# Performance work log

Hardware: AMD Instinct MI355X
Metric: run time of the kernel (lower is better)

## Reference

```python
import jax, jax.numpy as jnp
import numpy as np

EPS = 1e-6


def setup_inputs() -> dict:
    key = jax.random.key(0)
    ks = jax.random.split(key, 7)
    T, B, D, n, r = 512, 32, 1024, 1024, 8
    x = jax.random.normal(ks[0], (T, B, D), dtype=jnp.float32)
    # xavier_uniform-like init for weights
    def xavier(k, shape):
        fan_in, fan_out = shape[1], shape[0]
        a = float(np.sqrt(6.0 / (fan_in + fan_out)))
        return jax.random.uniform(k, shape, dtype=jnp.float32, minval=-a, maxval=a)
    W_k = xavier(ks[1], (n, D))
    W_v = xavier(ks[2], (n, D))
    W_q = xavier(ks[3], (n, D))
    W_kr = xavier(ks[4], (r, n))
    U0 = jnp.zeros((B, n, r), dtype=jnp.float32)
    V0 = jax.random.normal(ks[5], (B, n, r), dtype=jnp.float32) * 0.01
    return {"x": x, "W_k": W_k, "W_v": W_v, "W_q": W_q, "W_kr": W_kr, "U0": U0, "V0": V0}


def reference(x, W_k, W_v, W_q, W_kr, U0, V0):
    # x: [T, B, D]; state S = U @ V^T with U,V: [B, n, r]
    k = jnp.einsum('tbd,nd->tbn', x, W_k)
    v = jnp.einsum('tbd,nd->tbn', x, W_v)
    q = jnp.einsum('tbd,nd->tbn', x, W_q)
    V = V0  # V is never updated in the recurrence

    def step(U, kvq):
        k_t, v_t, q_t = kvq  # each [B, n]
        k_norm = k_t / (jnp.linalg.norm(k_t, axis=-1, keepdims=True) + EPS)
        Vtk = jnp.einsum('bnr,bn->br', V, k_norm)
        retrieved = jnp.einsum('bnr,br->bn', U, Vtk)
        delta = v_t - retrieved
        k_r = k_norm @ W_kr.T  # [B, r]
        U_new = jnp.tanh(U + delta[:, :, None] * k_r[:, None, :])
        Vtq = jnp.einsum('bnr,bn->br', V, q_t)
        Sq = jnp.einsum('bnr,br->bn', U_new, Vtq)
        out = Sq * jax.nn.silu(Sq)
        return U_new, out

    U_final, output = jax.lax.scan(step, U0, (k, v, q))
    return output, (U_final, V)
```

## Files before the change

kernel.cpp:

```cpp
#include <hip/hip_runtime.h>
#include <hip/hip_bf16.h>

typedef __attribute__((ext_vector_type(8))) short short8;
typedef __attribute__((ext_vector_type(4))) short short4v;
typedef __attribute__((ext_vector_type(4))) float f32x4;
typedef __attribute__((ext_vector_type(2))) float f32x2;
typedef unsigned short u16;

__device__ inline float b2f(u16 u) {
    unsigned int i = ((unsigned int)u) << 16;
    float f; __builtin_memcpy(&f, &i, 4); return f;
}
__device__ inline u16 f2b(float f) {
    unsigned int i; __builtin_memcpy(&i, &f, 4);
    unsigned int r = (i + 0x7FFFu + ((i >> 16) & 1u)) >> 16;
    return (u16)r;
}

__device__ inline float xsum32(float x) {
    unsigned u; __builtin_memcpy(&u, &x, 4);
    auto r = __builtin_amdgcn_permlane32_swap(u, u, false, false);
    unsigned s0 = r[0], s1 = r[1];
    float f0, f1; __builtin_memcpy(&f0, &s0, 4); __builtin_memcpy(&f1, &s1, 4);
    return f0 + f1;
}

__device__ inline float xsum16(float x) {
#if __has_builtin(__builtin_amdgcn_permlane16_swap)
    unsigned u; __builtin_memcpy(&u, &x, 4);
    auto r = __builtin_amdgcn_permlane16_swap(u, u, false, false);
    unsigned s0 = r[0], s1 = r[1];
    float f0, f1; __builtin_memcpy(&f0, &s0, 4); __builtin_memcpy(&f1, &s1, 4);
    return f0 + f1;
#else
    return x + __shfl_xor(x, 16, 64);
#endif
}

#define GLDS(g, l) __builtin_amdgcn_global_load_lds( \
    (const __attribute__((address_space(1))) void*)(g), \
    (__attribute__((address_space(3))) void*)(l), 16, 0, 0)

#define KWAIT(N) asm volatile("s_waitcnt lgkmcnt(0)\n\t" \
                              "s_waitcnt vmcnt(" #N ")\n\t" \
                              "s_barrier" ::: "memory")

__global__ __launch_bounds__(256) void cvt_k(const float* __restrict__ src,
                                             u16* __restrict__ dst, int n4)
{
    const int i = blockIdx.x * blockDim.x + threadIdx.x;
    if (i < n4) {
        const f32x4 v = ((const f32x4*)src)[i];
        short4v o;
        o.x = (short)f2b(v.x); o.y = (short)f2b(v.y);
        o.z = (short)f2b(v.z); o.w = (short)f2b(v.w);
        ((short4v*)dst)[i] = o;
    }
}

__global__ __launch_bounds__(256) void vT_k(const float* __restrict__ V0,
                                            float* __restrict__ V0T)
{
    const int gid = blockIdx.x * 256 + threadIdx.x;
    const int b = gid >> 9, j = (gid >> 6) & 7, n0 = (gid & 63) * 16;
    const float* src = V0 + (long)b * 8192 + (long)n0 * 8 + j;
    float* dst = V0T + (long)b * 8192 + (long)j * 1024 + n0;
#pragma unroll
    for (int i = 0; i < 16; i += 4) {
        f32x4 o = { src[(i + 0) * 8], src[(i + 1) * 8],
                    src[(i + 2) * 8], src[(i + 3) * 8] };
        *(f32x4*)(dst + i) = o;
    }
}

__global__ __launch_bounds__(256) void foldq_k(const float* __restrict__ V0T,
                                               const float* __restrict__ Wq,
                                               float* __restrict__ Aqp)
{
    const int bid = blockIdx.x;
    const int b  = bid >> 5;
    const int kc = (bid >> 2) & 7;
    const int dg = bid & 3;
    const int tid = threadIdx.x;
    const int d = dg * 256 + tid;

    __shared__ float rs[8][128];
    {
        const int j = tid >> 5, nn = (tid & 31) * 4;
        *(f32x4*)&rs[j][nn] =
            *(const f32x4*)(V0T + (long)b * 8192 + j * 1024 + kc * 128 + nn);
    }
    __syncthreads();

    float acc[8];
#pragma unroll
    for (int r = 0; r < 8; ++r) acc[r] = 0.f;

    const float* wp = Wq + (long)(kc * 128) * 1024 + d;
#pragma unroll 4
    for (int nb = 0; nb < 32; ++nb) {
        const float w0 = wp[0];
        const float w1 = wp[1024];
        const float w2 = wp[2048];
        const float w3 = wp[3072];
        wp += 4096;
#pragma unroll
        for (int r = 0; r < 8; ++r) {
            const f32x4 rv = *(const f32x4*)&rs[r][nb * 4];
            float a = acc[r];
            a = fmaf(rv.x, w0, a);
            a = fmaf(rv.y, w1, a);
            a = fmaf(rv.z, w2, a);
            a = fmaf(rv.w, w3, a);
            acc[r] = a;
        }
    }

#pragma unroll
    for (int r = 0; r < 8; ++r)
        Aqp[(long)kc * 262144 + (long)(b * 8 + r) * 1024 + d] = acc[r];
}

__global__ __launch_bounds__(256) void redq_k(const float* __restrict__ Aqp,
                                              float* __restrict__ Aq)
{
    const int i = blockIdx.x * 256 + threadIdx.x;
    f32x4 s = ((const f32x4*)Aqp)[i];
#pragma unroll
    for (int kc = 1; kc < 8; ++kc) {
        const f32x4 p = ((const f32x4*)Aqp)[(long)kc * 65536 + i];
        s.x += p.x; s.y += p.y; s.z += p.z; s.w += p.w;
    }
    ((f32x4*)Aq)[i] = s;
}

__global__ __launch_bounds__(512) void gemm256_kv(
    const u16* __restrict__ Xbf, const u16* __restrict__ Wbf,
    u16* __restrict__ Ko, u16* __restrict__ Vo)
{
    __shared__ u16 lds[65536];

    const int bid = blockIdx.x;
    const int swz = (bid & 7) * 64 + (bid >> 3);
    const int bm = swz >> 3, bnx = swz & 7;
    const int widx = bnx >> 2;
    const int nbase = (bnx & 3) * 256;
    const int m0 = bm * 256;
    const u16* Wp = Wbf + (long)widx * 1048576;
    u16* O = (widx == 0) ? Ko : Vo;

    const int tid = threadIdx.x;
    const int w = tid >> 6;
    const int lane = tid & 63;
    const int wm = (w >> 2) * 128;
    const int wn = (w & 3) * 64;
    const int ln = lane & 15, qd = lane >> 4;

    const int q8 = lane >> 3, s8 = lane & 7;
    const int cc = s8 ^ q8;
    const u16* p0; const u16* p1; const u16* p2; const u16* p3;
    {
        auto mk = [&](int l) -> const u16* {
            const int r = l * 64 + w * 8 + q8;
            return (cc < 4)
                ? (Xbf + (long)(m0 + r) * 1024 + cc * 8)
                : (Wp  + (long)(nbase + r) * 1024 + (cc - 4) * 8);
        };
        p0 = mk(0); p1 = mk(1); p2 = mk(2); p3 = mk(3);
    }

    int aoff[8], boff[4];
#pragma unroll
    for (int mf = 0; mf < 8; ++mf) {
        const int ro = wm + mf * 16 + ln;
        aoff[mf] = ro * 128 + ((qd ^ (ro & 7)) * 16);
    }
#pragma unroll
    for (int nf = 0; nf < 4; ++nf) {
        const int rb = wn + nf * 16 + ln;
        boff[nf] = rb * 128 + (((4 + qd) ^ (rb & 7)) * 16);
    }

    f32x4 acc[8][4];
#pragma unroll
    for (int i = 0; i < 8; ++i)
#pragma unroll
        for (int j = 0; j < 4; ++j) acc[i][j] = (f32x4){0.f, 0.f, 0.f, 0.f};

#pragma unroll
    for (int tt = 0; tt < 3; ++tt) {
        char* db = (char*)lds + tt * 32768 + w * 1024;
        GLDS(p0, db);
        GLDS(p1, db + 8192);
        GLDS(p2, db + 16384);
        GLDS(p3, db + 24576);
        p0 += 32; p1 += 32; p2 += 32; p3 += 32;
    }
    KWAIT(8);

    for (int t = 0; t < 32; ++t) {
        const char* bb = (const char*)lds + (t & 3) * 32768;
        short8 a[8], bfr[4];
#pragma unroll
        for (int mf = 0; mf < 4; ++mf) a[mf] = *(const short8*)(bb + aoff[mf]);
#pragma unroll
        for (int nf = 0; nf < 4; ++nf) bfr[nf] = *(const short8*)(bb + boff[nf]);
        if (t < 29) {
            char* db = (char*)lds + ((t + 3) & 3) * 32768 + w * 1024;
            GLDS(p0, db);
            GLDS(p1, db + 8192);
            p0 += 32; p1 += 32;
        }
        __builtin_amdgcn_s_setprio(1);
#pragma unroll
        for (int mf = 0; mf < 4; ++mf)
#pragma unroll
            for (int nf = 0; nf < 4; ++nf)
                acc[mf][nf] = __builtin_amdgcn_mfma_f32_16x16x32_bf16(
                    a[mf], bfr[nf], acc[mf][nf], 0, 0, 0);
        __builtin_amdgcn_s_setprio(0);
#pragma unroll
        for (int mf = 4; mf < 8; ++mf) a[mf] = *(const short8*)(bb + aoff[mf]);
        if (t < 29) {
            char* db = (char*)lds + ((t + 3) & 3) * 32768 + w * 1024;
            GLDS(p2, db + 16384);
            GLDS(p3, db + 24576);
            p2 += 32; p3 += 32;
        }
        __builtin_amdgcn_s_setprio(1);
#pragma unroll
        for (int mf = 4; mf < 8; ++mf)
#pragma unroll
            for (int nf = 0; nf < 4; ++nf)
                acc[mf][nf] = __builtin_amdgcn_mfma_f32_16x16x32_bf16(
                    a[mf], bfr[nf], acc[mf][nf], 0, 0, 0);
        __builtin_amdgcn_s_setprio(0);
        if (t < 29)       KWAIT(8);
        else if (t == 29) KWAIT(4);
        else if (t == 30) KWAIT(0);
    }

#pragma unroll
    for (int mf = 0; mf < 8; ++mf) {
#pragma unroll
        for (int nf = 0; nf < 4; ++nf) {
            const int r0 = m0 + wm + mf * 16 + qd * 4;
            const int c  = nbase + wn + nf * 16 + ln;
#pragma unroll
            for (int r = 0; r < 4; ++r)
                O[(long)(r0 + r) * 1024 + c] = f2b(acc[mf][nf][r]);
        }
    }
}

__global__ __launch_bounds__(256) void scal_k(
    const u16* __restrict__ K, const u16* __restrict__ X,
    const float* __restrict__ V0T, const float* __restrict__ Wkr,
    const float* __restrict__ Aq, float* __restrict__ S)
{
    const int b  = blockIdx.x & 31;
    const int t0 = (blockIdx.x >> 5) * 4;
    const int tid = threadIdx.x;
    const int j = tid & 7, c = tid >> 3;
    const int n0 = c * 32;

    f32x4 vv[8], ww[8], aqv[8];
    {
        const f32x4* vp = (const f32x4*)(V0T + (long)b * 8192 + (long)j * 1024 + n0);
        const f32x4* wp = (const f32x4*)(Wkr + (long)j * 1024 + n0);
        const f32x4* ap = (const f32x4*)(Aq + (long)(b * 8 + j) * 1024 + n0);
#pragma unroll
        for (int i = 0; i < 8; i++) { vv[i] = vp[i]; ww[i] = wp[i]; aqv[i] = ap[i]; }
    }

    float avk[4], akr[4], avq[4], ass[4];
#pragma unroll
    for (int dt = 0; dt < 4; dt++) { avk[dt] = akr[dt] = avq[dt] = ass[dt] = 0.f; }

#pragma unroll
    for (int dt = 0; dt < 4; dt++) {
        const long m = (long)(t0 + dt) * 32 + b;
        const short8* kp = (const short8*)(K + m * 1024 + n0);
        const short8* xp = (const short8*)(X + m * 1024 + n0);
#pragma unroll
        for (int i = 0; i < 4; i++) {
            const short8 kb = kp[i], xb = xp[i];
#pragma unroll
            for (int e = 0; e < 8; e++) {
                const int idx = i * 8 + e;
                const float kv = b2f((u16)kb[e]);
                const float xv = b2f((u16)xb[e]);
                const float vj = vv[idx >> 2][idx & 3];
                const float wj = ww[idx >> 2][idx & 3];
                const float aj = aqv[idx >> 2][idx & 3];
                avk[dt] = fmaf(vj, kv, avk[dt]);
                akr[dt] = fmaf(wj, kv, akr[dt]);
                avq[dt] = fmaf(aj, xv, avq[dt]);
                ass[dt] = fmaf(kv, kv, ass[dt]);
            }
        }
    }

    __shared__ float red[4][4][3][8];
    __shared__ float ssr[4][4];
    const int wave = tid >> 6, lane = tid & 63;
#pragma unroll
    for (int dt = 0; dt < 4; dt++) {
        float a = avk[dt], k2 = akr[dt], q = avq[dt], s = ass[dt];
#pragma unroll
        for (int off = 8; off < 64; off <<= 1) {
            a  += __shfl_xor(a,  off, 64);
            k2 += __shfl_xor(k2, off, 64);
            q  += __shfl_xor(q,  off, 64);
            s  += __shfl_xor(s,  off, 64);
        }
        if (lane < 8) {
            red[wave][dt][0][lane] = a;
            red[wave][dt][1][lane] = k2;
            red[wave][dt][2][lane] = q;
        }
        if (lane == 0) ssr[wave][dt] = s;
    }
    __syncthreads();
    if (tid < 128) {
        const int dt = tid >> 5, rr = tid & 31;
        if (rr < 24) {
            const int v = rr >> 3, jj = rr & 7;
            float s = red[0][dt][v][jj] + red[1][dt][v][jj] +
                      red[2][dt][v][jj] + red[3][dt][v][jj];
            if (v != 2) {
                const float n2 = ssr[0][dt] + ssr[1][dt] + ssr[2][dt] + ssr[3][dt];
                const float inv = 1.0f / (sqrtf(n2) + 1e-6f);
                s *= (v == 0) ? (0.5f * inv) : (2.0f * inv);
            } else {
                s *= 0.5f;
            }
            S[((long)b * 512 + t0 + dt) * 32 + v * 8 + jj] = s;
        }
    }
}

__global__ __launch_bounds__(256) void scan_k(
    const u16* __restrict__ Vbuf, const float* __restrict__ S,
    const float* __restrict__ U0, float* __restrict__ outp,
    float* __restrict__ Ufin)
{
    const int b = blockIdx.x >> 4;
    const int chunk = blockIdx.x & 15;
    const int wave = threadIdx.x >> 6, lane = threadIdx.x & 63;
    const int rq = lane >> 4;
    const int nl = lane & 15;
    const int n = chunk * 64 + wave * 16 + nl;
    const int so = rq * 2;

    float U[2];
    {
        const float* u0 = U0 + ((long)b * 1024 + n) * 8 + so;
        U[0] = 2.0f * u0[0];
        U[1] = 2.0f * u0[1];
    }

    const u16* vp0 = Vbuf + (long)b * 1024 + n;
    u16 vnx[16];
#pragma unroll
    for (int i = 0; i < 16; i++) vnx[i] = vp0[(long)i * 32768];

    const float* Sp = S + (long)b * 16384 + so;
    f32x2 sb[8][3];
#pragma unroll
    for (int s = 0; s < 8; ++s)
#pragma unroll
        for (int v = 0; v < 3; ++v)
            sb[s][v] = *(const f32x2*)(Sp + s * 32 + v * 8);

    float* op = outp + (long)b * 1024 + n;

    for (int t0 = 0; t0 < 512; t0 += 16) {
        float vcur[16];
#pragma unroll
        for (int i = 0; i < 16; i++) vcur[i] = b2f(vnx[i]);
        const int tn = (t0 + 16 < 512) ? (t0 + 16) : t0;
#pragma unroll
        for (int i = 0; i < 16; i++) vnx[i] = vp0[(long)(tn + i) * 32768];

#pragma unroll
        for (int i = 0; i < 16; i++) {
            const int t = t0 + i;
            const int slot = i & 7;
            const f32x2 a = sb[slot][0], Kk = sb[slot][1], Qq = sb[slot][2];

            const float pr = fmaf(U[0], a.x, U[1] * a.y);
            const float ret = xsum32(xsum16(pr));
            const float delta = vcur[i] - ret;

            const float x0 = fmaf(delta, Kk.x, U[0]);
            const float x1 = fmaf(delta, Kk.y, U[1]);
            const float e0 = __expf(x0);
            const float e1 = __expf(x1);
            const float u0n = fmaf(-4.0f, __builtin_amdgcn_rcpf(e0 + 1.0f), 2.0f);
            const float u1n = fmaf(-4.0f, __builtin_amdgcn_rcpf(e1 + 1.0f), 2.0f);
            U[0] = u0n; U[1] = u1n;

            const float sqp = fmaf(u1n, Qq.y, u0n * Qq.x);

            const int tf = (t + 8 < 512) ? (t + 8) : 511;
#pragma unroll
            for (int v = 0; v < 3; ++v)
                sb[slot][v] = *(const f32x2*)(Sp + tf * 32 + v * 8);

            const float Sq = xsum32(xsum16(sqp));
            const float sg = __builtin_amdgcn_rcpf(1.0f + __expf(-Sq));
            const float o = Sq * Sq * sg;
            if (rq == 0) op[(long)t * 32768] = o;
        }
    }

    *(f32x2*)(Ufin + ((long)b * 1024 + n) * 8 + so) =
        (f32x2){0.5f * U[0], 0.5f * U[1]};
}

__global__ __launch_bounds__(256) void vcopy_k(const float* __restrict__ src,
                                               float* __restrict__ dst)
{
    const int i = blockIdx.x * blockDim.x + threadIdx.x;
    ((f32x4*)dst)[i] = ((const f32x4*)src)[i];
}

extern "C" void kernel_launch(void* const* d_in, const int* in_sizes, int n_in,
                              void* d_out, int out_size, void* d_ws, size_t ws_size,
                              hipStream_t stream)
{
    const float* x   = (const float*)d_in[0];
    const float* Wk  = (const float*)d_in[1];
    const float* Wv  = (const float*)d_in[2];
    const float* Wq  = (const float*)d_in[3];
    const float* Wkr = (const float*)d_in[4];
    const float* U0  = (const float*)d_in[5];
    const float* V0  = (const float*)d_in[6];
    float* out = (float*)d_out;

    char* ws = (char*)d_ws;
    u16*   Xbf = (u16*)(ws);
    u16*   Wbf = (u16*)(ws + 33554432);
    u16*   Kb  = (u16*)(ws + 39845888);
    u16*   Vb  = (u16*)(ws + 73400320);
    float* Aq  = (float*)(ws + 106954752);
    float* Aqp = (float*)(ws + 108003328);
    float* Sc  = (float*)(ws + 140509184);
    float* V0T = (float*)(ws + 142606336);

    cvt_k<<<16384, 256, 0, stream>>>(x,  Xbf,               4194304);
    cvt_k<<<1024,  256, 0, stream>>>(Wk, Wbf,                262144);
    cvt_k<<<1024,  256, 0, stream>>>(Wv, Wbf + 1048576,      262144);
    vT_k <<<64,    256, 0, stream>>>(V0, V0T);
    foldq_k<<<1024, 256, 0, stream>>>(V0T, Wq, Aqp);
    redq_k <<<256, 256, 0, stream>>>(Aqp, Aq);

    gemm256_kv<<<512, 512, 0, stream>>>(Xbf, Wbf, Kb, Vb);
    scal_k  <<<4096, 256, 0, stream>>>(Kb, Xbf, V0T, Wkr, Aq, Sc);
    scan_k  <<<512, 256, 0, stream>>>(Vb, Sc, U0, out, out + 16777216);
    vcopy_k <<<256, 256, 0, stream>>>(V0, out + 17039360);
}
```

Baseline: 425.4 us.

## Give each scan thread all 8 rank entries and fold log2e into scales

The recurrent scan kernel now assigns one thread per state row n, so each thread holds all 8 rank components of U. This removes the cross-lane permlane reductions that were on the serial per-timestep critical path, and the launch shrinks to 64-thread blocks. Scale constants are rewritten to include log2(e) so the tanh and sigmoid can use exp2 directly, with the scaling folded into the precomputed S coefficients. In exchange, each thread does 4x more transcendental work per step, the block count stays at 512 single-wave blocks (lower occupancy), and register pressure from 48 buffered float4 values rises.

```diff
diff --git a/kernel.cpp b/kernel.cpp
--- a/kernel.cpp
+++ b/kernel.cpp
@@ -7,6 +7,11 @@
 typedef __attribute__((ext_vector_type(2))) float f32x2;
 typedef unsigned short u16;
 
+#define CL   1.44269504088896340736f
+#define C2L  2.88539008177792681472f
+#define C4L  5.77078016355585362944f
+#define C0L  0.34657359027997264311f
+
 __device__ inline float b2f(u16 u) {
     unsigned int i = ((unsigned int)u) << 16;
     float f; __builtin_memcpy(&f, &i, 4); return f;
@@ -15,26 +20,6 @@
     unsigned int i; __builtin_memcpy(&i, &f, 4);
     unsigned int r = (i + 0x7FFFu + ((i >> 16) & 1u)) >> 16;
     return (u16)r;
-}
-
-__device__ inline float xsum32(float x) {
-    unsigned u; __builtin_memcpy(&u, &x, 4);
-    auto r = __builtin_amdgcn_permlane32_swap(u, u, false, false);
-    unsigned s0 = r[0], s1 = r[1];
-    float f0, f1; __builtin_memcpy(&f0, &s0, 4); __builtin_memcpy(&f1, &s1, 4);
-    return f0 + f1;
-}
-
-__device__ inline float xsum16(float x) {
-#if __has_builtin(__builtin_amdgcn_permlane16_swap)
-    unsigned u; __builtin_memcpy(&u, &x, 4);
-    auto r = __builtin_amdgcn_permlane16_swap(u, u, false, false);
-    unsigned s0 = r[0], s1 = r[1];
-    float f0, f1; __builtin_memcpy(&f0, &s0, 4); __builtin_memcpy(&f1, &s1, 4);
-    return f0 + f1;
-#else
-    return x + __shfl_xor(x, 16, 64);
-#endif
 }
 
 #define GLDS(g, l) __builtin_amdgcn_global_load_lds( \
@@ -331,33 +316,30 @@
             if (v != 2) {
                 const float n2 = ssr[0][dt] + ssr[1][dt] + ssr[2][dt] + ssr[3][dt];
                 const float inv = 1.0f / (sqrtf(n2) + 1e-6f);
-                s *= (v == 0) ? (0.5f * inv) : (2.0f * inv);
+                s *= (v == 0) ? (C0L * inv) : (C2L * inv);
             } else {
-                s *= 0.5f;
+                s *= C0L;
             }
             S[((long)b * 512 + t0 + dt) * 32 + v * 8 + jj] = s;
         }
     }
 }
 
-__global__ __launch_bounds__(256) void scan_k(
+__global__ __launch_bounds__(64) void scan_k(
     const u16* __restrict__ Vbuf, const float* __restrict__ S,
     const float* __restrict__ U0, float* __restrict__ outp,
     float* __restrict__ Ufin)
 {
     const int b = blockIdx.x >> 4;
     const int chunk = blockIdx.x & 15;
-    const int wave = threadIdx.x >> 6, lane = threadIdx.x & 63;
-    const int rq = lane >> 4;
-    const int nl = lane & 15;
-    const int n = chunk * 64 + wave * 16 + nl;
-    const int so = rq * 2;
-
-    float U[2];
+    const int n = chunk * 64 + threadIdx.x;
+
+    float W[8];
     {
-        const float* u0 = U0 + ((long)b * 1024 + n) * 8 + so;
-        U[0] = 2.0f * u0[0];
-        U[1] = 2.0f * u0[1];
+        const f32x4 u0a = *(const f32x4*)(U0 + ((long)b * 1024 + n) * 8);
+        const f32x4 u0b = *(const f32x4*)(U0 + ((long)b * 1024 + n) * 8 + 4);
+        W[0] = C2L * u0a.x; W[1] = C2L * u0a.y; W[2] = C2L * u0a.z; W[3] = C2L * u0a.w;
+        W[4] = C2L * u0b.x; W[5] = C2L * u0b.y; W[6] = C2L * u0b.z; W[7] = C2L * u0b.w;
     }
 
     const u16* vp0 = Vbuf + (long)b * 1024 + n;
@@ -365,13 +347,13 @@
 #pragma unroll
     for (int i = 0; i < 16; i++) vnx[i] = vp0[(long)i * 32768];
 
-    const float* Sp = S + (long)b * 16384 + so;
-    f32x2 sb[8][3];
+    const f32x4* Srow = (const f32x4*)(S + (long)b * 16384);
+    f32x4 sb[8][6];
 #pragma unroll
     for (int s = 0; s < 8; ++s)
 #pragma unroll
-        for (int v = 0; v < 3; ++v)
-            sb[s][v] = *(const f32x2*)(Sp + s * 32 + v * 8);
+        for (int k = 0; k < 6; ++k)
+            sb[s][k] = Srow[s * 8 + k];
 
     float* op = outp + (long)b * 1024 + n;
 
@@ -387,36 +369,48 @@
         for (int i = 0; i < 16; i++) {
             const int t = t0 + i;
             const int slot = i & 7;
-            const f32x2 a = sb[slot][0], Kk = sb[slot][1], Qq = sb[slot][2];
-
-            const float pr = fmaf(U[0], a.x, U[1] * a.y);
-            const float ret = xsum32(xsum16(pr));
+            const f32x4 a0 = sb[slot][0], a1 = sb[slot][1];
+            const f32x4 k0 = sb[slot][2], k1 = sb[slot][3];
+            const f32x4 q0 = sb[slot][4], q1 = sb[slot][5];
+
+            const float r01 = fmaf(W[0], a0.x, W[1] * a0.y);
+            const float r23 = fmaf(W[2], a0.z, W[3] * a0.w);
+            const float r45 = fmaf(W[4], a1.x, W[5] * a1.y);
+            const float r67 = fmaf(W[6], a1.z, W[7] * a1.w);
+            const float ret = (r01 + r23) + (r45 + r67);
             const float delta = vcur[i] - ret;
 
-            const float x0 = fmaf(delta, Kk.x, U[0]);
-            const float x1 = fmaf(delta, Kk.y, U[1]);
-            const float e0 = __expf(x0);
-            const float e1 = __expf(x1);
-            const float u0n = fmaf(-4.0f, __builtin_amdgcn_rcpf(e0 + 1.0f), 2.0f);
-            const float u1n = fmaf(-4.0f, __builtin_amdgcn_rcpf(e1 + 1.0f), 2.0f);
-            U[0] = u0n; U[1] = u1n;
-
-            const float sqp = fmaf(u1n, Qq.y, u0n * Qq.x);
+            const float kr[8] = {k0.x, k0.y, k0.z, k0.w, k1.x, k1.y, k1.z, k1.w};
+            const float vq[8] = {q0.x, q0.y, q0.z, q0.w, q1.x, q1.y, q1.z, q1.w};
+
+            float s0 = 0.f, s1 = 0.f;
+#pragma unroll
+            for (int j = 0; j < 8; j++) {
+                const float xx = fmaf(delta, kr[j], W[j]);
+                const float e  = __builtin_amdgcn_exp2f(xx);
+                const float rc = __builtin_amdgcn_rcpf(e + 1.0f);
+                const float uw = fmaf(-C4L, rc, C2L);
+                W[j] = uw;
+                if (j & 1) s1 = fmaf(uw, vq[j], s1);
+                else       s0 = fmaf(uw, vq[j], s0);
+            }
+            const float Sq = s0 + s1;
 
             const int tf = (t + 8 < 512) ? (t + 8) : 511;
 #pragma unroll
-            for (int v = 0; v < 3; ++v)
-                sb[slot][v] = *(const f32x2*)(Sp + tf * 32 + v * 8);
-
-            const float Sq = xsum32(xsum16(sqp));
-            const float sg = __builtin_amdgcn_rcpf(1.0f + __expf(-Sq));
-            const float o = Sq * Sq * sg;
-            if (rq == 0) op[(long)t * 32768] = o;
-        }
-    }
-
-    *(f32x2*)(Ufin + ((long)b * 1024 + n) * 8 + so) =
-        (f32x2){0.5f * U[0], 0.5f * U[1]};
+            for (int k = 0; k < 6; ++k) sb[slot][k] = Srow[tf * 8 + k];
+
+            const float eg = __builtin_amdgcn_exp2f(-CL * Sq);
+            const float sg = __builtin_amdgcn_rcpf(1.0f + eg);
+            op[(long)t * 32768] = Sq * Sq * sg;
+        }
+    }
+
+    {
+        float* uf = Ufin + ((long)b * 1024 + n) * 8;
+        *(f32x4*)(uf)     = (f32x4){C0L * W[0], C0L * W[1], C0L * W[2], C0L * W[3]};
+        *(f32x4*)(uf + 4) = (f32x4){C0L * W[4], C0L * W[5], C0L * W[6], C0L * W[7]};
+    }
 }
 
 __global__ __launch_bounds__(256) void vcopy_k(const float* __restrict__ src,
@@ -458,6 +452,6 @@
 
     gemm256_kv<<<512, 512, 0, stream>>>(Xbf, Wbf, Kb, Vb);
     scal_k  <<<4096, 256, 0, stream>>>(Kb, Xbf, V0T, Wkr, Aq, Sc);
-    scan_k  <<<512, 256, 0, stream>>>(Vb, Sc, U0, out, out + 16777216);
+    scan_k  <<<512, 64, 0, stream>>>(Vb, Sc, U0, out, out + 16777216);
     vcopy_k <<<256, 256, 0, stream>>>(V0, out + 17039360);
 }
```

New measurement: 523.3 us. 23.0% more time.
